# Kernel optimization log

Hardware: AMD Instinct MI355X
Metric: run time of the kernel (lower is better)

Reference implementation:

```python
import jax, jax.numpy as jnp
import numpy as np

M, N, DIM, B = 64, 64, 512, 4096
SIGMA = max(M, N) / 2.0  # default sigma in BaseSOM.__init__


def setup_inputs() -> dict:
    key = jax.random.key(0)
    k1, k2 = jax.random.split(key)
    batch = jax.random.normal(k1, (B, DIM), dtype=jnp.float32)
    weights = jax.random.uniform(k2, (M * N, DIM), dtype=jnp.float32)
    # grid locations [(i, j) for i in range(M) for j in range(N)]
    ii, jj = jnp.meshgrid(jnp.arange(M), jnp.arange(N), indexing="ij")
    locations = jnp.stack([ii.reshape(-1), jj.reshape(-1)], axis=1).astype(jnp.int64)
    return {
        "batch": batch,
        "weights": weights,
        "locations": locations,
        "decay_rate": 1000,
        "it": 100,
    }


def reference(batch, weights, locations, decay_rate, it):
    # Squared Euclidean distances (argmin is identical to argmin of cdist p=2).
    x2 = jnp.sum(batch * batch, axis=1, keepdims=True)          # [B, 1]
    w2 = jnp.sum(weights * weights, axis=1)[None, :]            # [1, MN]
    d2 = x2 - 2.0 * (batch @ weights.T) + w2                    # [B, MN]
    bmu_indices = jnp.argmin(d2, axis=1)                        # [B]
    bmu_loc = locations[bmu_indices]                            # [B, 2]
    lr = jnp.exp(-jnp.float32(it) / jnp.float32(decay_rate))
    sigma_op = jnp.float32(SIGMA) * lr
    # [B, MN, 2] grid offsets -> squared grid distance [B, MN]
    diff = locations[None, :, :].astype(jnp.float32) - bmu_loc[:, None, :].astype(jnp.float32)
    dist_sq = jnp.sum(diff * diff, axis=2)
    return jnp.exp(-dist_sq / (sigma_op * sigma_op))
```

## Files before the change

### kernel.cpp

```cpp
#include <hip/hip_runtime.h>
#include <cfloat>

#define DIMK 512
#define MN   4096
#define BATCH 4096
#define NGRP 1024

typedef _Float16 half8_t __attribute__((ext_vector_type(8)));
typedef _Float16 half4_t __attribute__((ext_vector_type(4)));
typedef float f32x4 __attribute__((ext_vector_type(4)));

#define GLD16(gp, lp) __builtin_amdgcn_global_load_lds( \
    (const __attribute__((address_space(1))) void*)(gp), \
    (__attribute__((address_space(3))) void*)(lp), 16, 0, 0)

__global__ __launch_bounds__(256) void convert_kernel(
        const float* __restrict__ X, const float* __restrict__ W,
        _Float16* __restrict__ Xh, _Float16* __restrict__ Wh,
        float* __restrict__ w2, float* __restrict__ xnorm) {
    const int blk  = blockIdx.x;
    const int t    = threadIdx.x;
    const bool isW = blk >= 1024;
    const float* src = isW ? W : X;
    _Float16* dst  = isW ? Wh : Xh;
    const int rblk = isW ? blk - 1024 : blk;
    const size_t idx = (size_t)rblk * 2048 + (size_t)t * 8;

    float4 v0 = *(const float4*)(src + idx);
    float4 v1 = *(const float4*)(src + idx + 4);
    float v[8] = {v0.x, v0.y, v0.z, v0.w, v1.x, v1.y, v1.z, v1.w};
    half8_t hv;
    float s = 0.f;
#pragma unroll
    for (int e = 0; e < 8; e++) {
        s += v[e] * v[e];
        hv[e] = (_Float16)v[e];
    }
    *(half8_t*)(dst + idx) = hv;
#pragma unroll
    for (int o = 32; o > 0; o >>= 1) s += __shfl_down(s, o);
    if ((t & 63) == 0) {
        int row = rblk * 4 + (t >> 6);
        if (isW) w2[row] = s;
        else     xnorm[row] = __fsqrt_rn(s);
    }
}

#define MFMA_HALF(R) \
    do { \
        acc[(R)+0][0] = __builtin_amdgcn_mfma_f32_16x16x32_f16(ah0, bh0, acc[(R)+0][0], 0, 0, 0); \
        acc[(R)+0][1] = __builtin_amdgcn_mfma_f32_16x16x32_f16(ah0, bh1, acc[(R)+0][1], 0, 0, 0); \
        acc[(R)+0][2] = __builtin_amdgcn_mfma_f32_16x16x32_f16(ah0, bh2, acc[(R)+0][2], 0, 0, 0); \
        acc[(R)+0][3] = __builtin_amdgcn_mfma_f32_16x16x32_f16(ah0, bh3, acc[(R)+0][3], 0, 0, 0); \
        acc[(R)+1][0] = __builtin_amdgcn_mfma_f32_16x16x32_f16(ah1, bh0, acc[(R)+1][0], 0, 0, 0); \
        acc[(R)+1][1] = __builtin_amdgcn_mfma_f32_16x16x32_f16(ah1, bh1, acc[(R)+1][1], 0, 0, 0); \
        acc[(R)+1][2] = __builtin_amdgcn_mfma_f32_16x16x32_f16(ah1, bh2, acc[(R)+1][2], 0, 0, 0); \
        acc[(R)+1][3] = __builtin_amdgcn_mfma_f32_16x16x32_f16(ah1, bh3, acc[(R)+1][3], 0, 0, 0); \
        acc[(R)+2][0] = __builtin_amdgcn_mfma_f32_16x16x32_f16(ah2, bh0, acc[(R)+2][0], 0, 0, 0); \
        acc[(R)+2][1] = __builtin_amdgcn_mfma_f32_16x16x32_f16(ah2, bh1, acc[(R)+2][1], 0, 0, 0); \
        acc[(R)+2][2] = __builtin_amdgcn_mfma_f32_16x16x32_f16(ah2, bh2, acc[(R)+2][2], 0, 0, 0); \
        acc[(R)+2][3] = __builtin_amdgcn_mfma_f32_16x16x32_f16(ah2, bh3, acc[(R)+2][3], 0, 0, 0); \
        acc[(R)+3][0] = __builtin_amdgcn_mfma_f32_16x16x32_f16(ah3, bh0, acc[(R)+3][0], 0, 0, 0); \
        acc[(R)+3][1] = __builtin_amdgcn_mfma_f32_16x16x32_f16(ah3, bh1, acc[(R)+3][1], 0, 0, 0); \
        acc[(R)+3][2] = __builtin_amdgcn_mfma_f32_16x16x32_f16(ah3, bh2, acc[(R)+3][2], 0, 0, 0); \
        acc[(R)+3][3] = __builtin_amdgcn_mfma_f32_16x16x32_f16(ah3, bh3, acc[(R)+3][3], 0, 0, 0); \
    } while (0)

#define PHASE_TAIL(R) \
    do { \
        __builtin_amdgcn_s_barrier(); \
        asm volatile("s_waitcnt lgkmcnt(0)" ::: "memory"); \
        __builtin_amdgcn_sched_barrier(0); \
        __builtin_amdgcn_s_setprio(1); \
        MFMA_HALF(R); \
        __builtin_amdgcn_s_setprio(0); \
        __builtin_amdgcn_s_barrier(); \
    } while (0)

__global__ __launch_bounds__(512, 2) void score_kernel(
        const _Float16* __restrict__ Xh, const _Float16* __restrict__ Wh,
        const float* __restrict__ w2, float* __restrict__ Gm ) {
    __shared__ __align__(16) _Float16 lds[2][2][16384];

    const int t    = threadIdx.x;
    const int lane = t & 63;
    const int w    = t >> 6;
    const int wm   = w >> 2;
    const int wn   = w & 3;

    const int id  = blockIdx.y * 16 + blockIdx.x;
    const int xcd = id & 7;
    const int li  = id >> 3;
    const int bm  = (xcd >> 1) * 4 + (li >> 3);
    const int bn  = (xcd & 1) * 8 + (li & 7);
    const int m0  = bm * 256;
    const int n0  = bn * 256;

    const int srow = ((t >> 7) << 4) + (t & 15);
    const int skof = ((t >> 6) & 1) * 32 + ((t >> 4) & 3) * 8;
    const _Float16* gA = Xh + (size_t)(m0 + srow) * DIMK + skof;
    const _Float16* gB = Wh + (size_t)(n0 + srow) * DIMK + skof;
    const int ldst = t * 8;

#define STG_A(b, kt, c) GLD16(gA + (size_t)(c) * (64 * DIMK) + (kt) * 64, &lds[b][0][(c) * 4096 + ldst])
#define STG_B(b, kt, c) GLD16(gB + (size_t)(c) * (64 * DIMK) + (kt) * 64, &lds[b][1][(c) * 4096 + ldst])
#define LDA(b, rg, ks) (*(const half8_t*)(&lds[b][0][(rg) * 1024 + (ks) * 512 + lane * 8]))
#define LDB(b, rg, ks) (*(const half8_t*)(&lds[b][1][(rg) * 1024 + (ks) * 512 + lane * 8]))

    f32x4 acc[8][4];
#pragma unroll
    for (int i = 0; i < 8; i++)
#pragma unroll
        for (int j = 0; j < 4; j++) acc[i][j] = (f32x4){0.f, 0.f, 0.f, 0.f};

    STG_A(0, 0, 0); STG_A(0, 0, 1); STG_A(0, 0, 2); STG_A(0, 0, 3);
    STG_B(0, 0, 0); STG_B(0, 0, 1); STG_B(0, 0, 2); STG_B(0, 0, 3);

    half8_t ah0, ah1, ah2, ah3, bh0, bh1, bh2, bh3;

    for (int kt = 0; kt < 8; ++kt) {
        const int  b  = kt & 1;
        const int  nb = b ^ 1;
        const bool dn = kt < 7;

        if (dn) {
            STG_A(nb, kt + 1, 0); STG_A(nb, kt + 1, 1);
            asm volatile("s_waitcnt vmcnt(2)" ::: "memory");
        } else {
            asm volatile("s_waitcnt vmcnt(0)" ::: "memory");
        }
        __builtin_amdgcn_sched_barrier(0);
        __builtin_amdgcn_s_barrier();

        ah0 = LDA(b, wm * 8 + 0, 0); ah1 = LDA(b, wm * 8 + 1, 0);
        ah2 = LDA(b, wm * 8 + 2, 0); ah3 = LDA(b, wm * 8 + 3, 0);
        bh0 = LDB(b, wn * 4 + 0, 0); bh1 = LDB(b, wn * 4 + 1, 0);
        bh2 = LDB(b, wn * 4 + 2, 0); bh3 = LDB(b, wn * 4 + 3, 0);
        if (dn) { STG_A(nb, kt + 1, 2); STG_A(nb, kt + 1, 3); }
        PHASE_TAIL(0);

        ah0 = LDA(b, wm * 8 + 4, 0); ah1 = LDA(b, wm * 8 + 5, 0);
        ah2 = LDA(b, wm * 8 + 6, 0); ah3 = LDA(b, wm * 8 + 7, 0);
        if (dn) { STG_B(nb, kt + 1, 0); STG_B(nb, kt + 1, 1); }
        PHASE_TAIL(4);

        ah0 = LDA(b, wm * 8 + 0, 1); ah1 = LDA(b, wm * 8 + 1, 1);
        ah2 = LDA(b, wm * 8 + 2, 1); ah3 = LDA(b, wm * 8 + 3, 1);
        bh0 = LDB(b, wn * 4 + 0, 1); bh1 = LDB(b, wn * 4 + 1, 1);
        bh2 = LDB(b, wn * 4 + 2, 1); bh3 = LDB(b, wn * 4 + 3, 1);
        if (dn) { STG_B(nb, kt + 1, 2); STG_B(nb, kt + 1, 3); }
        PHASE_TAIL(0);

        ah0 = LDA(b, wm * 8 + 4, 1); ah1 = LDA(b, wm * 8 + 5, 1);
        ah2 = LDA(b, wm * 8 + 6, 1); ah3 = LDA(b, wm * 8 + 7, 1);
        PHASE_TAIL(4);
    }

    const int q   = lane >> 4;
    const int cl  = lane & 15;
    const int gb  = (n0 >> 2) + wn * 16;
    float w2v[4];
#pragma unroll
    for (int j = 0; j < 4; j++) w2v[j] = w2[n0 + wn * 64 + j * 16 + cl];
#pragma unroll
    for (int ai = 0; ai < 8; ai++)
#pragma unroll
        for (int v = 0; v < 4; v++) {
            const int row = m0 + wm * 128 + ai * 16 + q * 4 + v;
            _Float16* grow = (_Float16*)Gm + (size_t)row * 8192 + gb;
#pragma unroll
            for (int j = 0; j < 4; j++) {
                float s = w2v[j] - 2.0f * acc[ai][j][v];
                s = fminf(s, __shfl_xor(s, 1));
                s = fminf(s, __shfl_xor(s, 2));
                if ((cl & 3) == 0) grow[j * 4 + (cl >> 2)] = (_Float16)s;
            }
        }
}

__global__ __launch_bounds__(256) void epilogue_kernel(
        const float* __restrict__ w2, const float* __restrict__ xnorm,
        const float* __restrict__ X, const float* __restrict__ W,
        const int* __restrict__ decay_p, const int* __restrict__ it_p,
        float* out) {
    __shared__ float xs[512];
    __shared__ int   list[NGRP];
    __shared__ int   cnt;
    __shared__ float wmin[4];
    __shared__ float svv[4];
    __shared__ int   svi[4];
    __shared__ float tab[128];
    const int row  = blockIdx.x;
    const int t    = threadIdx.x;
    const int lane = t & 63;
    const int w    = t >> 6;

    {
        float2 xv = *(const float2*)(X + (size_t)row * DIMK + t * 2);
        xs[2 * t]     = xv.x;
        xs[2 * t + 1] = xv.y;
    }
    if (t == 0) cnt = 0;

    half4_t gmh = *((const half4_t*)((const _Float16*)out + (size_t)row * 8192) + t);
    float gme[4] = {(float)gmh[0], (float)gmh[1], (float)gmh[2], (float)gmh[3]};
    float g = fminf(fminf(gme[0], gme[1]), fminf(gme[2], gme[3]));
#pragma unroll
    for (int mask = 1; mask <= 32; mask <<= 1)
        g = fminf(g, __shfl_xor(g, mask));
    if (lane == 0) wmin[w] = g;
    __syncthreads();
    const float gmin = fminf(fminf(wmin[0], wmin[1]), fminf(wmin[2], wmin[3]));
    const float tau  = gmin + 2.0f * (0.0222f * xnorm[row] + 0.25f);

#pragma unroll
    for (int e = 0; e < 4; e++)
        if (gme[e] <= tau) list[atomicAdd(&cnt, 1)] = t * 4 + e;
    __syncthreads();
    const int total = cnt;

    float mbv = FLT_MAX;
    int   mbi = 0x7FFFFFFF;
    for (int idx = w; idx < total; idx += 4) {
        const int gid = list[idx];
#pragma unroll
        for (int cj = 0; cj < 4; cj++) {
            const int col = gid * 4 + cj;
            const float* wr = W + (size_t)col * DIMK;
            float p = 0.f;
#pragma unroll
            for (int e = 0; e < 8; e++) p += xs[lane * 8 + e] * wr[lane * 8 + e];
#pragma unroll
            for (int mask = 1; mask <= 32; mask <<= 1) p += __shfl_xor(p, mask);
            float s = w2[col] - 2.0f * p;
            if (s < mbv || (s == mbv && col < mbi)) { mbv = s; mbi = col; }
        }
    }
    if (lane == 0) { svv[w] = mbv; svi[w] = mbi; }
    __syncthreads();
    float sbv = svv[0]; int sbi = svi[0];
#pragma unroll
    for (int k = 1; k < 4; k++) {
        float s = svv[k]; int c = svi[k];
        if (s < sbv || (s == sbv && c < sbi)) { sbv = s; sbi = c; }
    }

    const float lr  = __expf(-(float)(*it_p) / (float)(*decay_p));
    const float so  = 32.0f * lr;
    const float inv = 1.0f / (so * so);
    const int rr = sbi >> 6, cc = sbi & 63;
    if (t < 64) {
        float d = (float)(t - rr);
        tab[t] = __expf(-d * d * inv);
    } else if (t < 128) {
        float d = (float)(t - 64 - cc);
        tab[t] = __expf(-d * d * inv);
    }
    __syncthreads();
    const float* er = tab;
    const float* ec = tab + 64;
    f32x4* orow = (f32x4*)(out + (size_t)row * 4096);
#pragma unroll
    for (int qq = 0; qq < 4; qq++) {
        int f  = qq * 256 + t;
        int i  = f >> 4;
        int j0 = (f & 15) * 4;
        float e = er[i];
        f32x4 o = {e * ec[j0], e * ec[j0 + 1], e * ec[j0 + 2], e * ec[j0 + 3]};
        __builtin_nontemporal_store(o, orow + f);
    }
}

extern "C" void kernel_launch(void* const* d_in, const int* in_sizes, int n_in,
                              void* d_out, int out_size, void* d_ws, size_t ws_size,
                              hipStream_t stream) {
    const float* X       = (const float*)d_in[0];
    const float* W       = (const float*)d_in[1];
    const int*   decay_p = (const int*)d_in[3];
    const int*   it_p    = (const int*)d_in[4];
    float* out = (float*)d_out;

    _Float16* Xh = (_Float16*)d_ws;
    _Float16* Wh = Xh + (size_t)BATCH * DIMK;
    float*    w2 = (float*)(Wh + (size_t)MN * DIMK);
    float*    xn = w2 + MN;

    convert_kernel<<<2048, 256, 0, stream>>>(X, W, Xh, Wh, w2, xn);
    score_kernel<<<dim3(16, 16), 512, 0, stream>>>(Xh, Wh, w2, out);
    epilogue_kernel<<<BATCH, 256, 0, stream>>>(w2, xn, X, W, decay_p, it_p, out);
}
```

Baseline: 134.6 us.

## Switch GEMM main loop to 4-stage K=32 pipeline with fewer barriers

Restructures the score GEMM main loop. It moves from 2 LDS buffers of K=64 to 4 buffers of K=32, with loads issued 3 stages ahead. Each iteration now has a single workgroup barrier instead of four per half-tile, and uses split lgkmcnt waits so the second MFMA group overlaps the remaining LDS reads. The aim is deeper global-to-LDS prefetch and less barrier stall, at the cost of more loop iterations and a tighter vmcnt accounting that must stay correct.

```diff
diff --git a/kernel.cpp b/kernel.cpp
--- a/kernel.cpp
+++ b/kernel.cpp
@@ -46,41 +46,30 @@
     }
 }
 
-#define MFMA_HALF(R) \
+#define MFMA16(A0, A1, A2, A3, R) \
     do { \
-        acc[(R)+0][0] = __builtin_amdgcn_mfma_f32_16x16x32_f16(ah0, bh0, acc[(R)+0][0], 0, 0, 0); \
-        acc[(R)+0][1] = __builtin_amdgcn_mfma_f32_16x16x32_f16(ah0, bh1, acc[(R)+0][1], 0, 0, 0); \
-        acc[(R)+0][2] = __builtin_amdgcn_mfma_f32_16x16x32_f16(ah0, bh2, acc[(R)+0][2], 0, 0, 0); \
-        acc[(R)+0][3] = __builtin_amdgcn_mfma_f32_16x16x32_f16(ah0, bh3, acc[(R)+0][3], 0, 0, 0); \
-        acc[(R)+1][0] = __builtin_amdgcn_mfma_f32_16x16x32_f16(ah1, bh0, acc[(R)+1][0], 0, 0, 0); \
-        acc[(R)+1][1] = __builtin_amdgcn_mfma_f32_16x16x32_f16(ah1, bh1, acc[(R)+1][1], 0, 0, 0); \
-        acc[(R)+1][2] = __builtin_amdgcn_mfma_f32_16x16x32_f16(ah1, bh2, acc[(R)+1][2], 0, 0, 0); \
-        acc[(R)+1][3] = __builtin_amdgcn_mfma_f32_16x16x32_f16(ah1, bh3, acc[(R)+1][3], 0, 0, 0); \
-        acc[(R)+2][0] = __builtin_amdgcn_mfma_f32_16x16x32_f16(ah2, bh0, acc[(R)+2][0], 0, 0, 0); \
-        acc[(R)+2][1] = __builtin_amdgcn_mfma_f32_16x16x32_f16(ah2, bh1, acc[(R)+2][1], 0, 0, 0); \
-        acc[(R)+2][2] = __builtin_amdgcn_mfma_f32_16x16x32_f16(ah2, bh2, acc[(R)+2][2], 0, 0, 0); \
-        acc[(R)+2][3] = __builtin_amdgcn_mfma_f32_16x16x32_f16(ah2, bh3, acc[(R)+2][3], 0, 0, 0); \
-        acc[(R)+3][0] = __builtin_amdgcn_mfma_f32_16x16x32_f16(ah3, bh0, acc[(R)+3][0], 0, 0, 0); \
-        acc[(R)+3][1] = __builtin_amdgcn_mfma_f32_16x16x32_f16(ah3, bh1, acc[(R)+3][1], 0, 0, 0); \
-        acc[(R)+3][2] = __builtin_amdgcn_mfma_f32_16x16x32_f16(ah3, bh2, acc[(R)+3][2], 0, 0, 0); \
-        acc[(R)+3][3] = __builtin_amdgcn_mfma_f32_16x16x32_f16(ah3, bh3, acc[(R)+3][3], 0, 0, 0); \
-    } while (0)
-
-#define PHASE_TAIL(R) \
-    do { \
-        __builtin_amdgcn_s_barrier(); \
-        asm volatile("s_waitcnt lgkmcnt(0)" ::: "memory"); \
-        __builtin_amdgcn_sched_barrier(0); \
-        __builtin_amdgcn_s_setprio(1); \
-        MFMA_HALF(R); \
-        __builtin_amdgcn_s_setprio(0); \
-        __builtin_amdgcn_s_barrier(); \
+        acc[(R)+0][0] = __builtin_amdgcn_mfma_f32_16x16x32_f16(A0, b0, acc[(R)+0][0], 0, 0, 0); \
+        acc[(R)+0][1] = __builtin_amdgcn_mfma_f32_16x16x32_f16(A0, b1, acc[(R)+0][1], 0, 0, 0); \
+        acc[(R)+0][2] = __builtin_amdgcn_mfma_f32_16x16x32_f16(A0, b2, acc[(R)+0][2], 0, 0, 0); \
+        acc[(R)+0][3] = __builtin_amdgcn_mfma_f32_16x16x32_f16(A0, b3, acc[(R)+0][3], 0, 0, 0); \
+        acc[(R)+1][0] = __builtin_amdgcn_mfma_f32_16x16x32_f16(A1, b0, acc[(R)+1][0], 0, 0, 0); \
+        acc[(R)+1][1] = __builtin_amdgcn_mfma_f32_16x16x32_f16(A1, b1, acc[(R)+1][1], 0, 0, 0); \
+        acc[(R)+1][2] = __builtin_amdgcn_mfma_f32_16x16x32_f16(A1, b2, acc[(R)+1][2], 0, 0, 0); \
+        acc[(R)+1][3] = __builtin_amdgcn_mfma_f32_16x16x32_f16(A1, b3, acc[(R)+1][3], 0, 0, 0); \
+        acc[(R)+2][0] = __builtin_amdgcn_mfma_f32_16x16x32_f16(A2, b0, acc[(R)+2][0], 0, 0, 0); \
+        acc[(R)+2][1] = __builtin_amdgcn_mfma_f32_16x16x32_f16(A2, b1, acc[(R)+2][1], 0, 0, 0); \
+        acc[(R)+2][2] = __builtin_amdgcn_mfma_f32_16x16x32_f16(A2, b2, acc[(R)+2][2], 0, 0, 0); \
+        acc[(R)+2][3] = __builtin_amdgcn_mfma_f32_16x16x32_f16(A2, b3, acc[(R)+2][3], 0, 0, 0); \
+        acc[(R)+3][0] = __builtin_amdgcn_mfma_f32_16x16x32_f16(A3, b0, acc[(R)+3][0], 0, 0, 0); \
+        acc[(R)+3][1] = __builtin_amdgcn_mfma_f32_16x16x32_f16(A3, b1, acc[(R)+3][1], 0, 0, 0); \
+        acc[(R)+3][2] = __builtin_amdgcn_mfma_f32_16x16x32_f16(A3, b2, acc[(R)+3][2], 0, 0, 0); \
+        acc[(R)+3][3] = __builtin_amdgcn_mfma_f32_16x16x32_f16(A3, b3, acc[(R)+3][3], 0, 0, 0); \
     } while (0)
 
 __global__ __launch_bounds__(512, 2) void score_kernel(
         const _Float16* __restrict__ Xh, const _Float16* __restrict__ Wh,
         const float* __restrict__ w2, float* __restrict__ Gm ) {
-    __shared__ __align__(16) _Float16 lds[2][2][16384];
+    __shared__ __align__(16) _Float16 lds[4][2][8192];
 
     const int t    = threadIdx.x;
     const int lane = t & 63;
@@ -96,16 +85,16 @@
     const int m0  = bm * 256;
     const int n0  = bn * 256;
 
-    const int srow = ((t >> 7) << 4) + (t & 15);
-    const int skof = ((t >> 6) & 1) * 32 + ((t >> 4) & 3) * 8;
+    const int srow = (t >> 6) * 16 + (t & 15);
+    const int skof = ((t >> 4) & 3) * 8;
     const _Float16* gA = Xh + (size_t)(m0 + srow) * DIMK + skof;
     const _Float16* gB = Wh + (size_t)(n0 + srow) * DIMK + skof;
     const int ldst = t * 8;
 
-#define STG_A(b, kt, c) GLD16(gA + (size_t)(c) * (64 * DIMK) + (kt) * 64, &lds[b][0][(c) * 4096 + ldst])
-#define STG_B(b, kt, c) GLD16(gB + (size_t)(c) * (64 * DIMK) + (kt) * 64, &lds[b][1][(c) * 4096 + ldst])
-#define LDA(b, rg, ks) (*(const half8_t*)(&lds[b][0][(rg) * 1024 + (ks) * 512 + lane * 8]))
-#define LDB(b, rg, ks) (*(const half8_t*)(&lds[b][1][(rg) * 1024 + (ks) * 512 + lane * 8]))
+#define STG_A(bf, kt, c) GLD16(gA + (size_t)(c) * (128 * DIMK) + (kt) * 32, &lds[bf][0][(c) * 4096 + ldst])
+#define STG_B(bf, kt, c) GLD16(gB + (size_t)(c) * (128 * DIMK) + (kt) * 32, &lds[bf][1][(c) * 4096 + ldst])
+#define LDA(bf, rg) (*(const half8_t*)(&lds[bf][0][(rg) * 512 + lane * 8]))
+#define LDB(bf, rg) (*(const half8_t*)(&lds[bf][1][(rg) * 512 + lane * 8]))
 
     f32x4 acc[8][4];
 #pragma unroll
@@ -113,47 +102,43 @@
 #pragma unroll
         for (int j = 0; j < 4; j++) acc[i][j] = (f32x4){0.f, 0.f, 0.f, 0.f};
 
-    STG_A(0, 0, 0); STG_A(0, 0, 1); STG_A(0, 0, 2); STG_A(0, 0, 3);
-    STG_B(0, 0, 0); STG_B(0, 0, 1); STG_B(0, 0, 2); STG_B(0, 0, 3);
-
-    half8_t ah0, ah1, ah2, ah3, bh0, bh1, bh2, bh3;
-
-    for (int kt = 0; kt < 8; ++kt) {
-        const int  b  = kt & 1;
-        const int  nb = b ^ 1;
-        const bool dn = kt < 7;
-
-        if (dn) {
-            STG_A(nb, kt + 1, 0); STG_A(nb, kt + 1, 1);
-            asm volatile("s_waitcnt vmcnt(2)" ::: "memory");
-        } else {
-            asm volatile("s_waitcnt vmcnt(0)" ::: "memory");
-        }
+    STG_A(0, 0, 0); STG_A(0, 0, 1); STG_B(0, 0, 0); STG_B(0, 0, 1);
+    STG_A(1, 1, 0); STG_A(1, 1, 1); STG_B(1, 1, 0); STG_B(1, 1, 1);
+    STG_A(2, 2, 0); STG_A(2, 2, 1); STG_B(2, 2, 0); STG_B(2, 2, 1);
+
+#pragma unroll
+    for (int kt = 0; kt < 16; ++kt) {
+        const int bf = kt & 3;
+        const int nb = (kt + 3) & 3;
+
+        if (kt <= 13)      { asm volatile("s_waitcnt vmcnt(8)" ::: "memory"); }
+        else if (kt == 14) { asm volatile("s_waitcnt vmcnt(4)" ::: "memory"); }
+        else               { asm volatile("s_waitcnt vmcnt(0)" ::: "memory"); }
         __builtin_amdgcn_sched_barrier(0);
         __builtin_amdgcn_s_barrier();
 
-        ah0 = LDA(b, wm * 8 + 0, 0); ah1 = LDA(b, wm * 8 + 1, 0);
-        ah2 = LDA(b, wm * 8 + 2, 0); ah3 = LDA(b, wm * 8 + 3, 0);
-        bh0 = LDB(b, wn * 4 + 0, 0); bh1 = LDB(b, wn * 4 + 1, 0);
-        bh2 = LDB(b, wn * 4 + 2, 0); bh3 = LDB(b, wn * 4 + 3, 0);
-        if (dn) { STG_A(nb, kt + 1, 2); STG_A(nb, kt + 1, 3); }
-        PHASE_TAIL(0);
-
-        ah0 = LDA(b, wm * 8 + 4, 0); ah1 = LDA(b, wm * 8 + 5, 0);
-        ah2 = LDA(b, wm * 8 + 6, 0); ah3 = LDA(b, wm * 8 + 7, 0);
-        if (dn) { STG_B(nb, kt + 1, 0); STG_B(nb, kt + 1, 1); }
-        PHASE_TAIL(4);
-
-        ah0 = LDA(b, wm * 8 + 0, 1); ah1 = LDA(b, wm * 8 + 1, 1);
-        ah2 = LDA(b, wm * 8 + 2, 1); ah3 = LDA(b, wm * 8 + 3, 1);
-        bh0 = LDB(b, wn * 4 + 0, 1); bh1 = LDB(b, wn * 4 + 1, 1);
-        bh2 = LDB(b, wn * 4 + 2, 1); bh3 = LDB(b, wn * 4 + 3, 1);
-        if (dn) { STG_B(nb, kt + 1, 2); STG_B(nb, kt + 1, 3); }
-        PHASE_TAIL(0);
-
-        ah0 = LDA(b, wm * 8 + 4, 1); ah1 = LDA(b, wm * 8 + 5, 1);
-        ah2 = LDA(b, wm * 8 + 6, 1); ah3 = LDA(b, wm * 8 + 7, 1);
-        PHASE_TAIL(4);
+        if (kt <= 12) { STG_A(nb, kt + 3, 0); STG_A(nb, kt + 3, 1); }
+
+        half8_t a0 = LDA(bf, wm * 8 + 0), a1 = LDA(bf, wm * 8 + 1);
+        half8_t a2 = LDA(bf, wm * 8 + 2), a3 = LDA(bf, wm * 8 + 3);
+        half8_t b0 = LDB(bf, wn * 4 + 0), b1 = LDB(bf, wn * 4 + 1);
+        half8_t b2 = LDB(bf, wn * 4 + 2), b3 = LDB(bf, wn * 4 + 3);
+        half8_t a4 = LDA(bf, wm * 8 + 4), a5 = LDA(bf, wm * 8 + 5);
+        half8_t a6 = LDA(bf, wm * 8 + 6), a7 = LDA(bf, wm * 8 + 7);
+
+        if (kt <= 12) { STG_B(nb, kt + 3, 0); STG_B(nb, kt + 3, 1); }
+
+        asm volatile("s_waitcnt lgkmcnt(4)" ::: "memory");
+        __builtin_amdgcn_sched_barrier(0);
+        __builtin_amdgcn_s_setprio(1);
+        MFMA16(a0, a1, a2, a3, 0);
+        __builtin_amdgcn_s_setprio(0);
+
+        asm volatile("s_waitcnt lgkmcnt(0)" ::: "memory");
+        __builtin_amdgcn_sched_barrier(0);
+        __builtin_amdgcn_s_setprio(1);
+        MFMA16(a4, a5, a6, a7, 4);
+        __builtin_amdgcn_s_setprio(0);
     }
 
     const int q   = lane >> 4;
```

After: 135.5 us. Within noise of the previous version (+0.7%).
